# Optimization experiments

Hardware: AMD Instinct MI355X
Metric: run time of the kernel (lower is better)

The kernel has to match this reference:

```python
import jax, jax.numpy as jnp
import numpy as np

TOP_K_FRACTION = 0.1


def setup_inputs() -> dict:
    key = jax.random.key(0)
    k1, k2, k3 = jax.random.split(key, 3)
    B, H, S, D = 2, 12, 1024, 64
    q = jax.random.normal(k1, (B, H, S, D), dtype=jnp.float32)
    k = jax.random.normal(k2, (B, H, S, D), dtype=jnp.float32)
    v = jax.random.normal(k3, (B, H, S, D), dtype=jnp.float32)
    mask = jnp.zeros((B, 1, 1, S), dtype=jnp.float32)
    return {"q": q, "k": k, "v": v, "mask": mask}


def reference(q, k, v, mask):
    B, H, S, D = q.shape
    k_precise = max(1, int(S * TOP_K_FRACTION))
    # binary (sign) approximation of attention scores; detached like torch
    q_bin = jnp.sign(jax.lax.stop_gradient(q))
    k_bin = jnp.sign(jax.lax.stop_gradient(k))
    approx_scores = jnp.einsum('bhsd,bhtd->bhst', q_bin, k_bin) / D  # [B,H,S,S]
    _, topk_idx = jax.lax.top_k(approx_scores, k_precise)  # [B,H,S,kp]
    # gather top-k keys/values per query: [B,H,S,kp,D]
    k_gathered = jnp.take_along_axis(k[:, :, None, :, :], topk_idx[..., None], axis=3)
    v_gathered = jnp.take_along_axis(v[:, :, None, :, :], topk_idx[..., None], axis=3)
    scale = np.float32(1.0 / np.sqrt(D))
    precise_scores = jnp.einsum('bhsd,bhskd->bhsk', q, k_gathered) * scale
    # gather mask along key positions: mask [B,1,1,S] -> [B,H,S,kp]
    mask_gathered = jnp.take_along_axis(
        jnp.broadcast_to(mask, (B, H, S, S)), topk_idx, axis=-1)
    precise_scores = precise_scores + mask_gathered
    precise_probs = jax.nn.softmax(precise_scores, axis=-1)
    attn_output = jnp.einsum('bhsk,bhskd->bhsd', precise_probs, v_gathered)
    return attn_output
```

## Files before the change

### kernel.cpp

```cpp
#include <hip/hip_runtime.h>
#include <hip/hip_fp16.h>
#include <cstdint>

#define BB 2
#define HH 12
#define SS 1024
#define DD 64
#define KP 102
#define QPB 4

typedef _Float16 half2v __attribute__((ext_vector_type(2)));
typedef _Float16 half8v __attribute__((ext_vector_type(8)));

template <int CTRL>
__device__ __forceinline__ float dpp_f(float x) {
    return __builtin_bit_cast(float,
        __builtin_amdgcn_update_dpp(0, __builtin_bit_cast(int, x), CTRL, 0xF, 0xF, false));
}
__device__ __forceinline__ float readlane_f(float x, int l) {
    return __builtin_bit_cast(float,
        __builtin_amdgcn_readlane(__builtin_bit_cast(int, x), l));
}
__device__ __forceinline__ float group8_sum(float x) {
    x += dpp_f<0xB1>(x);
    x += dpp_f<0x4E>(x);
    x += dpp_f<0x141>(x);
    return x;
}
__device__ __forceinline__ float wave_sum_f32(float x) {
    x += dpp_f<0xB1>(x);
    x += dpp_f<0x4E>(x);
    x += dpp_f<0x141>(x);
    x += dpp_f<0x140>(x);
    return (readlane_f(x, 0) + readlane_f(x, 16))
         + (readlane_f(x, 32) + readlane_f(x, 48));
}
__device__ __forceinline__ float wave_max_f32(float x) {
    x = fmaxf(x, dpp_f<0xB1>(x));
    x = fmaxf(x, dpp_f<0x4E>(x));
    x = fmaxf(x, dpp_f<0x141>(x));
    x = fmaxf(x, dpp_f<0x140>(x));
    return fmaxf(fmaxf(readlane_f(x, 0), readlane_f(x, 16)),
                 fmaxf(readlane_f(x, 32), readlane_f(x, 48)));
}

__global__ __launch_bounds__(256) void pack_k_kernel(
    const float* __restrict__ k, unsigned long long* __restrict__ kbits,
    _Float16* __restrict__ kh)
{
    int row  = (int)((blockIdx.x * 256 + threadIdx.x) >> 6);
    int lane = (int)(threadIdx.x & 63);
    if (row >= BB * HH * SS) return;
    float kv = k[(size_t)row * DD + lane];
    unsigned long long km = __ballot(kv > 0.0f);
    kh[(size_t)row * DD + lane] = (_Float16)kv;
    if (lane == 0) kbits[row] = km;
}

__global__ __launch_bounds__(256) void battn_kernel(
    const float* __restrict__ q, const _Float16* __restrict__ kh,
    const float* __restrict__ v, const float* __restrict__ mask,
    const unsigned long long* __restrict__ kbits,
    float* __restrict__ out)
{
    const int tid  = (int)threadIdx.x;
    const int w    = tid >> 6;
    const int lane = tid & 63;
    const int query = (int)blockIdx.x * QPB + w;
    const int bh    = query >> 10;
    const int b     = bh / HH;

    __shared__ int   sel_t[QPB][KP];
    __shared__ float sel_p[QPB][KP];

    const float qreg = q[(size_t)query * DD + lane];
    const unsigned long long qm = __ballot(qreg > 0.0f);

    const unsigned long long* kb = kbits + (size_t)bh * SS;
    int binv[16];
    #pragma unroll
    for (int j = 0; j < 16; ++j)
        binv[j] = 64 - __popcll(qm ^ kb[j * 64 + lane]);

    int lo = 0, hi = 65;
    #pragma unroll 1
    while (hi - lo > 1) {
        int mid = (lo + hi) >> 1;
        int c = 0;
        #pragma unroll
        for (int j = 0; j < 16; ++j)
            c += (int)__popcll(__ballot(binv[j] >= mid));
        if (c >= KP) lo = mid; else hi = mid;
    }
    const int binT = lo;
    int cgt = 0;
    #pragma unroll
    for (int j = 0; j < 16; ++j)
        cgt += (int)__popcll(__ballot(binv[j] > binT));
    const int need = KP - cgt;

    const unsigned long long lmask_lt = (lane == 0) ? 0ULL : (~0ULL >> (64 - lane));
    int base = 0, tie_base = 0;
    #pragma unroll
    for (int j = 0; j < 16; ++j) {
        bool isGt  = binv[j] > binT;
        bool isTie = (binv[j] == binT);
        unsigned long long tiem = __ballot(isTie);
        int rank = tie_base + (int)__popcll(tiem & lmask_lt);
        bool take = isGt || (isTie && rank < need);
        unsigned long long tm = __ballot(take);
        if (take)
            sel_t[w][base + (int)__popcll(tm & lmask_lt)] = j * 64 + lane;
        base     += (int)__popcll(tm);
        tie_base += (int)__popcll(tiem);
    }

    const int sub = lane & 7, g = lane >> 3;
    const float* qrow = q + (size_t)query * DD + sub * 8;
    half2v qh[4];
    #pragma unroll
    for (int d = 0; d < 4; ++d) {
        float2 f2 = *(const float2*)(qrow + d * 2);
        half2v h; h[0] = (_Float16)f2.x; h[1] = (_Float16)f2.y;
        qh[d] = h;
    }
    const _Float16* krows = kh + (size_t)bh * SS * DD;
    #pragma unroll 1
    for (int i0 = 0; i0 < KP; i0 += 8) {
        int i = i0 + g;
        bool valid = (i < KP);
        float partial = 0.0f;
        if (valid) {
            int t = sel_t[w][i];
            half8v kv8 = *(const half8v*)(krows + (size_t)t * DD + sub * 8);
            half2v k0; k0[0] = kv8[0]; k0[1] = kv8[1];
            half2v k1; k1[0] = kv8[2]; k1[1] = kv8[3];
            half2v k2; k2[0] = kv8[4]; k2[1] = kv8[5];
            half2v k3; k3[0] = kv8[6]; k3[1] = kv8[7];
            partial = __builtin_amdgcn_fdot2(qh[0], k0, partial, false);
            partial = __builtin_amdgcn_fdot2(qh[1], k1, partial, false);
            partial = __builtin_amdgcn_fdot2(qh[2], k2, partial, false);
            partial = __builtin_amdgcn_fdot2(qh[3], k3, partial, false);
        }
        partial = group8_sum(partial);
        if (valid && sub == 0)
            sel_p[w][i] = partial * 0.125f;
    }

    const float* maskrow = mask + (size_t)b * SS;
    const bool has2 = (lane < KP - 64);
    int   t0 = sel_t[w][lane];
    int   t1 = has2 ? sel_t[w][lane + 64] : 0;
    float p0 = sel_p[w][lane] + maskrow[t0];
    float p1 = has2 ? (sel_p[w][lane + 64] + maskrow[t1]) : -3.0e38f;
    float m  = wave_max_f32(fmaxf(p0, p1));
    float e0 = __expf(p0 - m);
    float e1 = has2 ? __expf(p1 - m) : 0.0f;
    float rinv = __frcp_rn(wave_sum_f32(e0 + e1));
    float w0 = e0 * rinv;
    float w1 = e1 * rinv;

    const float* vbase = v + (size_t)bh * SS * DD + lane;
    float acc0 = 0.0f, acc1 = 0.0f;
    #pragma unroll
    for (int i = 0; i < 64; i += 2) {
        int   ta = __builtin_amdgcn_readlane(t0, i);
        float pa = readlane_f(w0, i);
        int   tb = __builtin_amdgcn_readlane(t0, i + 1);
        float pb = readlane_f(w0, i + 1);
        acc0 = fmaf(pa, vbase[(size_t)ta * DD], acc0);
        acc1 = fmaf(pb, vbase[(size_t)tb * DD], acc1);
    }
    #pragma unroll
    for (int i = 0; i < KP - 64; i += 2) {
        int   ta = __builtin_amdgcn_readlane(t1, i);
        float pa = readlane_f(w1, i);
        int   tb = __builtin_amdgcn_readlane(t1, i + 1);
        float pb = readlane_f(w1, i + 1);
        acc0 = fmaf(pa, vbase[(size_t)ta * DD], acc0);
        acc1 = fmaf(pb, vbase[(size_t)tb * DD], acc1);
    }
    out[(size_t)query * DD + lane] = acc0 + acc1;
}

extern "C" void kernel_launch(void* const* d_in, const int* in_sizes, int n_in,
                              void* d_out, int out_size, void* d_ws, size_t ws_size,
                              hipStream_t stream) {
    const float* q    = (const float*)d_in[0];
    const float* k    = (const float*)d_in[1];
    const float* v    = (const float*)d_in[2];
    const float* mask = (const float*)d_in[3];
    float* out = (float*)d_out;

    const int rows = BB * HH * SS;
    unsigned long long* kbits = (unsigned long long*)d_ws;
    _Float16* kh = (_Float16*)((char*)d_ws + (size_t)rows * sizeof(unsigned long long));

    pack_k_kernel<<<(rows * 64 + 255) / 256, 256, 0, stream>>>(k, kbits, kh);
    battn_kernel<<<rows / QPB, 256, 0, stream>>>(q, kh, v, mask, kbits, out);
}
```

Baseline: 135.9 us.

## Pack V to fp16 and gather K/V rows with 8-wide vector loads

The pack kernel now also converts V to fp16. The PV stage switches from one key per lane-iteration with readlane broadcasts to 8 keys per iteration: each 8-lane group loads a half8 slice and the partial sums are reduced with xor shuffles before a float4 store. Selected indices and weights are passed between lanes with ds_bpermute instead of LDS reads, the 1/8 score scale is folded into q, the QK loop is fully unrolled, and launch bounds request higher occupancy. This cuts gathered V bytes and serial load latency, at the cost of fp16 rounding of V and an extra pass over V in the pack kernel.

```diff
diff --git a/kernel.cpp b/kernel.cpp
--- a/kernel.cpp
+++ b/kernel.cpp
@@ -7,6 +7,7 @@
 #define SS 1024
 #define DD 64
 #define KP 102
+#define KPAD 104
 #define QPB 4
 
 typedef _Float16 half2v __attribute__((ext_vector_type(2)));
@@ -20,6 +21,13 @@
 __device__ __forceinline__ float readlane_f(float x, int l) {
     return __builtin_bit_cast(float,
         __builtin_amdgcn_readlane(__builtin_bit_cast(int, x), l));
+}
+__device__ __forceinline__ int bperm_i(int addr4, int src) {
+    return __builtin_amdgcn_ds_bpermute(addr4, src);
+}
+__device__ __forceinline__ float bperm_f(int addr4, float src) {
+    return __builtin_bit_cast(float,
+        __builtin_amdgcn_ds_bpermute(addr4, __builtin_bit_cast(int, src)));
 }
 __device__ __forceinline__ float group8_sum(float x) {
     x += dpp_f<0xB1>(x);
@@ -44,22 +52,25 @@
                  fmaxf(readlane_f(x, 32), readlane_f(x, 48)));
 }
 
-__global__ __launch_bounds__(256) void pack_k_kernel(
-    const float* __restrict__ k, unsigned long long* __restrict__ kbits,
-    _Float16* __restrict__ kh)
+__global__ __launch_bounds__(256) void pack_kernel(
+    const float* __restrict__ k, const float* __restrict__ v,
+    unsigned long long* __restrict__ kbits,
+    _Float16* __restrict__ kh, _Float16* __restrict__ vh)
 {
     int row  = (int)((blockIdx.x * 256 + threadIdx.x) >> 6);
     int lane = (int)(threadIdx.x & 63);
     if (row >= BB * HH * SS) return;
     float kv = k[(size_t)row * DD + lane];
+    float vv = v[(size_t)row * DD + lane];
     unsigned long long km = __ballot(kv > 0.0f);
     kh[(size_t)row * DD + lane] = (_Float16)kv;
+    vh[(size_t)row * DD + lane] = (_Float16)vv;
     if (lane == 0) kbits[row] = km;
 }
 
-__global__ __launch_bounds__(256) void battn_kernel(
+__global__ __launch_bounds__(256, 4) void battn_kernel(
     const float* __restrict__ q, const _Float16* __restrict__ kh,
-    const float* __restrict__ v, const float* __restrict__ mask,
+    const _Float16* __restrict__ vh, const float* __restrict__ mask,
     const unsigned long long* __restrict__ kbits,
     float* __restrict__ out)
 {
@@ -70,8 +81,8 @@
     const int bh    = query >> 10;
     const int b     = bh / HH;
 
-    __shared__ int   sel_t[QPB][KP];
-    __shared__ float sel_p[QPB][KP];
+    __shared__ int   sel_t[QPB][KPAD];
+    __shared__ float sel_p[QPB][KPAD];
 
     const float qreg = q[(size_t)query * DD + lane];
     const unsigned long long qm = __ballot(qreg > 0.0f);
@@ -115,42 +126,38 @@
         tie_base += (int)__popcll(tiem);
     }
 
+    const int t0 = sel_t[w][lane];
+    const int t1 = (lane < KP - 64) ? sel_t[w][lane + 64] : 0;
+
     const int sub = lane & 7, g = lane >> 3;
     const float* qrow = q + (size_t)query * DD + sub * 8;
     half2v qh[4];
     #pragma unroll
     for (int d = 0; d < 4; ++d) {
         float2 f2 = *(const float2*)(qrow + d * 2);
-        half2v h; h[0] = (_Float16)f2.x; h[1] = (_Float16)f2.y;
+        half2v h; h[0] = (_Float16)(f2.x * 0.125f); h[1] = (_Float16)(f2.y * 0.125f);
         qh[d] = h;
     }
     const _Float16* krows = kh + (size_t)bh * SS * DD;
-    #pragma unroll 1
+    #pragma unroll
     for (int i0 = 0; i0 < KP; i0 += 8) {
-        int i = i0 + g;
-        bool valid = (i < KP);
-        float partial = 0.0f;
-        if (valid) {
-            int t = sel_t[w][i];
-            half8v kv8 = *(const half8v*)(krows + (size_t)t * DD + sub * 8);
-            half2v k0; k0[0] = kv8[0]; k0[1] = kv8[1];
-            half2v k1; k1[0] = kv8[2]; k1[1] = kv8[3];
-            half2v k2; k2[0] = kv8[4]; k2[1] = kv8[5];
-            half2v k3; k3[0] = kv8[6]; k3[1] = kv8[7];
-            partial = __builtin_amdgcn_fdot2(qh[0], k0, partial, false);
-            partial = __builtin_amdgcn_fdot2(qh[1], k1, partial, false);
-            partial = __builtin_amdgcn_fdot2(qh[2], k2, partial, false);
-            partial = __builtin_amdgcn_fdot2(qh[3], k3, partial, false);
-        }
+        const int addr = ((i0 & 63) + g) << 2;
+        int t = bperm_i(addr, (i0 < 64) ? t0 : t1);
+        half8v kv8 = *(const half8v*)(krows + (size_t)t * DD + sub * 8);
+        half2v k0; k0[0] = kv8[0]; k0[1] = kv8[1];
+        half2v k1; k1[0] = kv8[2]; k1[1] = kv8[3];
+        half2v k2; k2[0] = kv8[4]; k2[1] = kv8[5];
+        half2v k3; k3[0] = kv8[6]; k3[1] = kv8[7];
+        float partial = __builtin_amdgcn_fdot2(qh[0], k0, 0.0f, false);
+        partial = __builtin_amdgcn_fdot2(qh[1], k1, partial, false);
+        partial = __builtin_amdgcn_fdot2(qh[2], k2, partial, false);
+        partial = __builtin_amdgcn_fdot2(qh[3], k3, partial, false);
         partial = group8_sum(partial);
-        if (valid && sub == 0)
-            sel_p[w][i] = partial * 0.125f;
+        if (sub == 0) sel_p[w][i0 + g] = partial;
     }
 
     const float* maskrow = mask + (size_t)b * SS;
     const bool has2 = (lane < KP - 64);
-    int   t0 = sel_t[w][lane];
-    int   t1 = has2 ? sel_t[w][lane + 64] : 0;
     float p0 = sel_p[w][lane] + maskrow[t0];
     float p1 = has2 ? (sel_p[w][lane + 64] + maskrow[t1]) : -3.0e38f;
     float m  = wave_max_f32(fmaxf(p0, p1));
@@ -160,27 +167,33 @@
     float w0 = e0 * rinv;
     float w1 = e1 * rinv;
 
-    const float* vbase = v + (size_t)bh * SS * DD + lane;
-    float acc0 = 0.0f, acc1 = 0.0f;
-    #pragma unroll
-    for (int i = 0; i < 64; i += 2) {
-        int   ta = __builtin_amdgcn_readlane(t0, i);
-        float pa = readlane_f(w0, i);
-        int   tb = __builtin_amdgcn_readlane(t0, i + 1);
-        float pb = readlane_f(w0, i + 1);
-        acc0 = fmaf(pa, vbase[(size_t)ta * DD], acc0);
-        acc1 = fmaf(pb, vbase[(size_t)tb * DD], acc1);
-    }
-    #pragma unroll
-    for (int i = 0; i < KP - 64; i += 2) {
-        int   ta = __builtin_amdgcn_readlane(t1, i);
-        float pa = readlane_f(w1, i);
-        int   tb = __builtin_amdgcn_readlane(t1, i + 1);
-        float pb = readlane_f(w1, i + 1);
-        acc0 = fmaf(pa, vbase[(size_t)ta * DD], acc0);
-        acc1 = fmaf(pb, vbase[(size_t)tb * DD], acc1);
-    }
-    out[(size_t)query * DD + lane] = acc0 + acc1;
+    const _Float16* vrows = vh + (size_t)bh * SS * DD;
+    float acc[8] = {0.f, 0.f, 0.f, 0.f, 0.f, 0.f, 0.f, 0.f};
+    #pragma unroll
+    for (int i0 = 0; i0 < KP; i0 += 8) {
+        const int addr = ((i0 & 63) + g) << 2;
+        int   t  = bperm_i(addr, (i0 < 64) ? t0 : t1);
+        float wt = bperm_f(addr, (i0 < 64) ? w0 : w1);
+        half8v vv = *(const half8v*)(vrows + (size_t)t * DD + sub * 8);
+        #pragma unroll
+        for (int d = 0; d < 8; ++d)
+            acc[d] = fmaf(wt, (float)vv[d], acc[d]);
+    }
+    #pragma unroll
+    for (int d = 0; d < 8; ++d) {
+        float x = acc[d];
+        x += __shfl_xor(x, 8);
+        x += __shfl_xor(x, 16);
+        x += __shfl_xor(x, 32);
+        acc[d] = x;
+    }
+    if (lane < 8) {
+        float* orow = out + (size_t)query * DD + lane * 8;
+        float4 o0 = make_float4(acc[0], acc[1], acc[2], acc[3]);
+        float4 o1 = make_float4(acc[4], acc[5], acc[6], acc[7]);
+        *(float4*)orow       = o0;
+        *(float4*)(orow + 4) = o1;
+    }
 }
 
 extern "C" void kernel_launch(void* const* d_in, const int* in_sizes, int n_in,
@@ -195,7 +208,8 @@
     const int rows = BB * HH * SS;
     unsigned long long* kbits = (unsigned long long*)d_ws;
     _Float16* kh = (_Float16*)((char*)d_ws + (size_t)rows * sizeof(unsigned long long));
-
-    pack_k_kernel<<<(rows * 64 + 255) / 256, 256, 0, stream>>>(k, kbits, kh);
-    battn_kernel<<<rows / QPB, 256, 0, stream>>>(q, kh, v, mask, kbits, out);
-}
+    _Float16* vh = kh + (size_t)rows * DD;
+
+    pack_kernel<<<(rows * 64 + 255) / 256, 256, 0, stream>>>(k, v, kbits, kh, vh);
+    battn_kernel<<<rows / QPB, 256, 0, stream>>>(q, kh, vh, mask, kbits, out);
+}
```

New measurement: 120.2 us. 1.13x faster.
